# Performance work log

Hardware: AMD Instinct MI355X
Metric: run time of the kernel (lower is better)

Reference implementation:

```python
import jax, jax.numpy as jnp
import numpy as np


def _grid_sample_3d(vol, grid):
    """Trilinear 3D grid_sample, zero padding, align_corners=False (torch default).

    vol:  [B, C, D, H, W]
    grid: [B, P, 3] normalized coords in [-1, 1]; grid[...,0]->W axis,
          grid[...,1]->H axis, grid[...,2]->D axis (torch convention).
    returns [B, C, P]
    """
    B, C, D, H, W = vol.shape
    x = (grid[..., 0] + 1.0) * (W * 0.5) - 0.5
    y = (grid[..., 1] + 1.0) * (H * 0.5) - 0.5
    z = (grid[..., 2] + 1.0) * (D * 0.5) - 0.5
    x0, y0, z0 = jnp.floor(x), jnp.floor(y), jnp.floor(z)
    gather = jax.vmap(lambda v, zz, yy, xx: v[:, zz, yy, xx])  # per-batch gather -> [C, P]
    out = jnp.zeros((B, C, x.shape[1]), vol.dtype)
    for dz in (0.0, 1.0):
        for dy in (0.0, 1.0):
            for dx in (0.0, 1.0):
                xi, yi, zi = x0 + dx, y0 + dy, z0 + dz
                w = (1.0 - jnp.abs(x - xi)) * (1.0 - jnp.abs(y - yi)) * (1.0 - jnp.abs(z - zi))
                valid = (xi >= 0) & (xi < W) & (yi >= 0) & (yi < H) & (zi >= 0) & (zi < D)
                xc = jnp.clip(xi, 0, W - 1).astype(jnp.int32)
                yc = jnp.clip(yi, 0, H - 1).astype(jnp.int32)
                zc = jnp.clip(zi, 0, D - 1).astype(jnp.int32)
                vals = gather(vol, zc, yc, xc)  # [B, C, P]
                out = out + vals * jnp.where(valid, w, 0.0)[:, None, :]
    return out


def _offset_grid(xs, A, Wk):
    """xs: [N,3] sample points; A: [N,3,3]; Wk: [3,K] offset weights.
    Returns [N, K, 3] grid coords ordered (z_feat, y_feat, x_feat) as in the torch code."""
    off = jnp.einsum('nij,jk->nik', A, Wk)  # bmm with repeated weight -> [N,3,K]
    xf = xs[:, 2:3] + off[:, 0, :]
    yf = xs[:, 1:2] + off[:, 1, :]
    zf = xs[:, 0:1] + off[:, 2, :]
    return jnp.stack([zf, yf, xf], axis=-1)


def setup_inputs() -> dict:
    key = jax.random.key(0)
    k1, k2, k3, k4 = jax.random.split(key, 4)
    B, C, D, H, W = 2, 16, 96, 96, 96
    Feats, K = 512, 1024
    inp = jax.random.normal(k1, (B, C, D, H, W), jnp.float32)
    xyz_sample = jax.random.uniform(k2, (B, Feats, 3), jnp.float32, -1.0, 1.0)
    A = jax.random.normal(k3, (B * Feats, 3, 3), jnp.float32) * 0.1
    weight = jax.random.normal(k4, (6, K), jnp.float32) * 0.05  # xyz_off.weight
    return {"input": inp, "xyz_sample": xyz_sample, "A": A, "weight": weight}


def reference(input, xyz_sample, A, weight):
    B, Feats, _ = xyz_sample.shape
    C = input.shape[1]
    K = weight.shape[1]  # 1024
    xs = xyz_sample.reshape(B * Feats, 3)
    g1 = _offset_grid(xs, A, weight[:3]).reshape(B, Feats * K, 3)
    g2 = _offset_grid(xs, A, weight[3:]).reshape(B, Feats * K, 3)
    feats = _grid_sample_3d(input, g1) - _grid_sample_3d(input, g2)  # [B, C, Feats*K]
    return feats.reshape(B, C * Feats, K)
```

## Files before the change

### kernel.cpp

```cpp
#include <hip/hip_runtime.h>


#define NB 2
#define NC 16
#define NS 96
#define FEATS 512
#define NK 1024
#define KSPLIT 4
#define KSHIFT 2
#define KCHUNK (NK / KSPLIT)
#define PASSES (KCHUNK / 64)

#define TP 388

__device__ __forceinline__ unsigned int bfround(float f) {
  unsigned int u = __float_as_uint(f);
  return (u + 0x7fffu + ((u >> 16) & 1u)) >> 16;
}

__global__ __launch_bounds__(256) void transpose_bf16_kernel(
    const float* __restrict__ vol, unsigned short* __restrict__ volT) {
  int bid = blockIdx.x;
  int hq = bid % 24;
  int t = bid / 24;
  int d = t % NS;
  int b = t / NS;

  __shared__ float sm[NC * TP];
  int tid = threadIdx.x;

  const float4* v4 = (const float4*)vol;
#pragma unroll
  for (int j = 0; j < 6; j++) {
    int i = tid + 256 * j;
    int c = i / 96;
    int u = i - c * 96;
    size_t src = (size_t)((b * NC + c) * NS + d) * 2304 + hq * 96 + u;
    *(float4*)&sm[c * TP + u * 4] = v4[src];
  }
  __syncthreads();

  size_t dstb = ((size_t)(b * NS + d) * 9216 + (size_t)hq * 384) * NC;
#pragma unroll
  for (int j = 0; j < 3; j++) {
    int m = tid + 256 * j;
    int t16 = m >> 1;
    int ch = m & 1;
    unsigned int r[4];
#pragma unroll
    for (int q = 0; q < 4; q++) {
      float lo = sm[(ch * 8 + 2 * q) * TP + t16];
      float hi = sm[(ch * 8 + 2 * q + 1) * TP + t16];
      r[q] = bfround(lo) | (bfround(hi) << 16);
    }
    *(uint4*)(volT + dstb + (size_t)m * 8) = make_uint4(r[0], r[1], r[2], r[3]);
  }
}

__device__ __forceinline__ void tri_q_bf16(const unsigned short* __restrict__ vq,
                                           size_t bbase, float x, float y,
                                           float z, float sgn, float acc[4]) {
  float fx0 = floorf(x), fy0 = floorf(y), fz0 = floorf(z);
  int ix0 = (int)fx0, iy0 = (int)fy0, iz0 = (int)fz0;
  float tx = x - fx0, ty = y - fy0, tz = z - fz0;
  float wxa[2] = {1.0f - tx, tx};
  float wya[2] = {1.0f - ty, ty};
  float wza[2] = {1.0f - tz, tz};

#pragma unroll
  for (int dz = 0; dz < 2; dz++) {
    int zc = iz0 + dz;
    if ((unsigned)zc >= (unsigned)NS) continue;
#pragma unroll
    for (int dy = 0; dy < 2; dy++) {
      int yc = iy0 + dy;
      if ((unsigned)yc >= (unsigned)NS) continue;
      size_t rowb = bbase + ((size_t)zc * NS + yc) * (NS * NC);
      float wzy = sgn * wza[dz] * wya[dy];
#pragma unroll
      for (int dx = 0; dx < 2; dx++) {
        int xc = ix0 + dx;
        if ((unsigned)xc >= (unsigned)NS) continue;
        float w = wzy * wxa[dx];
        uint2 u = *(const uint2*)(vq + rowb + (size_t)xc * NC);
        acc[0] += w * __uint_as_float(u.x << 16);
        acc[1] += w * __uint_as_float(u.x & 0xffff0000u);
        acc[2] += w * __uint_as_float(u.y << 16);
        acc[3] += w * __uint_as_float(u.y & 0xffff0000u);
      }
    }
  }
}

__global__ __launch_bounds__(256) void sample_kernel_q(
    const unsigned short* __restrict__ volT,
    const float* __restrict__ xyz, const float* __restrict__ A,
    const float* __restrict__ weight, float* __restrict__ out) {
  __shared__ float wsm[6 * KCHUNK];

  int bid = blockIdx.x;
  int kseg = bid & (KSPLIT - 1);
  int n = bid >> KSHIFT;
  int b = n >> 9;
  int f = n & 511;
  int kbase = kseg * KCHUNK;

  for (int i = threadIdx.x; i < 6 * KCHUNK; i += 256)
    wsm[i] = weight[(i / KCHUNK) * NK + kbase + (i % KCHUNK)];

  const float* An = A + (size_t)n * 9;
  float a00 = An[0], a01 = An[1], a02 = An[2];
  float a10 = An[3], a11 = An[4], a12 = An[5];
  float a20 = An[6], a21 = An[7], a22 = An[8];
  const float* Xn = xyz + (size_t)n * 3;
  float bx = (Xn[0] + 1.0f) * 48.0f - 0.5f;
  float by = (Xn[1] + 1.0f) * 48.0f - 0.5f;
  float bz = (Xn[2] + 1.0f) * 48.0f - 0.5f;
  __syncthreads();

  int quad = threadIdx.x & 3;
  int ksub = threadIdx.x >> 2;
  const unsigned short* vq = volT + quad * 4;
  size_t bbase = (size_t)b * (NS * NS * NS * NC);
  size_t obase = (size_t)b * (NC * FEATS * NK) +
                 (size_t)(quad * 4) * (FEATS * NK) + (size_t)f * NK + kbase;

  for (int pass = 0; pass < PASSES; pass++) {
    int kl = pass * 64 + ksub;
    float w0 = wsm[kl];
    float w1 = wsm[KCHUNK + kl];
    float w2 = wsm[2 * KCHUNK + kl];
    float w3 = wsm[3 * KCHUNK + kl];
    float w4 = wsm[4 * KCHUNK + kl];
    float w5 = wsm[5 * KCHUNK + kl];

    float acc[4] = {0.0f, 0.0f, 0.0f, 0.0f};

    {
      float oz = a00 * w0 + a01 * w1 + a02 * w2;
      float oy = a10 * w0 + a11 * w1 + a12 * w2;
      float ox = a20 * w0 + a21 * w1 + a22 * w2;
      tri_q_bf16(vq, bbase, bx + ox * 48.0f, by + oy * 48.0f, bz + oz * 48.0f,
                 1.0f, acc);
    }
    {
      float oz = a00 * w3 + a01 * w4 + a02 * w5;
      float oy = a10 * w3 + a11 * w4 + a12 * w5;
      float ox = a20 * w3 + a21 * w4 + a22 * w5;
      tri_q_bf16(vq, bbase, bx + ox * 48.0f, by + oy * 48.0f, bz + oz * 48.0f,
                 -1.0f, acc);
    }

    size_t o = obase + kl;
    out[o] = acc[0];
    out[o + (size_t)(FEATS * NK)] = acc[1];
    out[o + 2 * (size_t)(FEATS * NK)] = acc[2];
    out[o + 3 * (size_t)(FEATS * NK)] = acc[3];
  }
}

__global__ __launch_bounds__(256) void sample_kernel_fallback(
    const float* __restrict__ vol, const float* __restrict__ xyz,
    const float* __restrict__ A, const float* __restrict__ weight,
    float* __restrict__ out) {
  int n = blockIdx.x;
  int b = n >> 9;
  int f = n & 511;
  const float* An = A + (size_t)n * 9;
  float a00 = An[0], a01 = An[1], a02 = An[2];
  float a10 = An[3], a11 = An[4], a12 = An[5];
  float a20 = An[6], a21 = An[7], a22 = An[8];
  const float* Xn = xyz + (size_t)n * 3;
  float bx = (Xn[0] + 1.0f) * 48.0f - 0.5f;
  float by = (Xn[1] + 1.0f) * 48.0f - 0.5f;
  float bz = (Xn[2] + 1.0f) * 48.0f - 0.5f;
  size_t obase = (size_t)b * (NC * FEATS * NK) + (size_t)f * NK;

  for (int k = threadIdx.x; k < NK; k += 256) {
    float w0 = weight[k], w1 = weight[NK + k], w2 = weight[2 * NK + k];
    float w3 = weight[3 * NK + k], w4 = weight[4 * NK + k],
          w5 = weight[5 * NK + k];
    float acc[NC];
#pragma unroll
    for (int c = 0; c < NC; c++) acc[c] = 0.0f;
    for (int g = 0; g < 2; g++) {
      float u0 = g ? w3 : w0, u1 = g ? w4 : w1, u2 = g ? w5 : w2;
      float sgn = g ? -1.0f : 1.0f;
      float oz = a00 * u0 + a01 * u1 + a02 * u2;
      float oy = a10 * u0 + a11 * u1 + a12 * u2;
      float ox = a20 * u0 + a21 * u1 + a22 * u2;
      float x = bx + ox * 48.0f, y = by + oy * 48.0f, z = bz + oz * 48.0f;
      float fx0 = floorf(x), fy0 = floorf(y), fz0 = floorf(z);
      int ix0 = (int)fx0, iy0 = (int)fy0, iz0 = (int)fz0;
      float tx = x - fx0, ty = y - fy0, tz = z - fz0;
      float wxa[2] = {1.0f - tx, tx}, wya[2] = {1.0f - ty, ty},
            wza[2] = {1.0f - tz, tz};
      for (int dz = 0; dz < 2; dz++) {
        int zc = iz0 + dz;
        if ((unsigned)zc >= (unsigned)NS) continue;
        for (int dy = 0; dy < 2; dy++) {
          int yc = iy0 + dy;
          if ((unsigned)yc >= (unsigned)NS) continue;
          for (int dx = 0; dx < 2; dx++) {
            int xc = ix0 + dx;
            if ((unsigned)xc >= (unsigned)NS) continue;
            float w = sgn * wza[dz] * wya[dy] * wxa[dx];
            size_t base = (size_t)b * NC * NS * NS * NS +
                          (size_t)zc * NS * NS + (size_t)yc * NS + xc;
#pragma unroll
            for (int c = 0; c < NC; c++)
              acc[c] += w * vol[base + (size_t)c * (NS * NS * NS)];
          }
        }
      }
    }
#pragma unroll
    for (int c = 0; c < NC; c++)
      out[obase + (size_t)c * (FEATS * NK) + k] = acc[c];
  }
}

extern "C" void kernel_launch(void* const* d_in, const int* in_sizes, int n_in,
                              void* d_out, int out_size, void* d_ws,
                              size_t ws_size, hipStream_t stream) {
  const float* vol    = (const float*)d_in[0];
  const float* xyz    = (const float*)d_in[1];
  const float* A      = (const float*)d_in[2];
  const float* weight = (const float*)d_in[3];
  float* out = (float*)d_out;

  const size_t volT_bytes =
      (size_t)NB * NC * NS * NS * NS * sizeof(unsigned short);

  if (ws_size >= volT_bytes) {
    unsigned short* volT = (unsigned short*)d_ws;
    transpose_bf16_kernel<<<NB * NS * 24, 256, 0, stream>>>(vol, volT);
    sample_kernel_q<<<NB * FEATS * KSPLIT, 256, 0, stream>>>(volT, xyz, A,
                                                             weight, out);
  } else {
    sample_kernel_fallback<<<NB * FEATS, 256, 0, stream>>>(vol, xyz, A, weight,
                                                           out);
  }
}
```

Before: 242.7 us.

## Replace full-volume bf16 transpose with per-block bounding-box LDS staging

```diff
diff --git a/kernel.cpp b/kernel.cpp
--- a/kernel.cpp
+++ b/kernel.cpp
@@ -10,56 +10,22 @@
 #define KSHIFT 2
 #define KCHUNK (NK / KSPLIT)
 #define PASSES (KCHUNK / 64)
-
-#define TP 388
+#define BOX 8
+#define VOXPAD 10
+#define PLANE (NS * NS)
+#define VOLC ((size_t)NS * NS * NS)
 
 __device__ __forceinline__ unsigned int bfround(float f) {
   unsigned int u = __float_as_uint(f);
   return (u + 0x7fffu + ((u >> 16) & 1u)) >> 16;
 }
-
-__global__ __launch_bounds__(256) void transpose_bf16_kernel(
-    const float* __restrict__ vol, unsigned short* __restrict__ volT) {
-  int bid = blockIdx.x;
-  int hq = bid % 24;
-  int t = bid / 24;
-  int d = t % NS;
-  int b = t / NS;
-
-  __shared__ float sm[NC * TP];
-  int tid = threadIdx.x;
-
-  const float4* v4 = (const float4*)vol;
-#pragma unroll
-  for (int j = 0; j < 6; j++) {
-    int i = tid + 256 * j;
-    int c = i / 96;
-    int u = i - c * 96;
-    size_t src = (size_t)((b * NC + c) * NS + d) * 2304 + hq * 96 + u;
-    *(float4*)&sm[c * TP + u * 4] = v4[src];
-  }
-  __syncthreads();
-
-  size_t dstb = ((size_t)(b * NS + d) * 9216 + (size_t)hq * 384) * NC;
-#pragma unroll
-  for (int j = 0; j < 3; j++) {
-    int m = tid + 256 * j;
-    int t16 = m >> 1;
-    int ch = m & 1;
-    unsigned int r[4];
-#pragma unroll
-    for (int q = 0; q < 4; q++) {
-      float lo = sm[(ch * 8 + 2 * q) * TP + t16];
-      float hi = sm[(ch * 8 + 2 * q + 1) * TP + t16];
-      r[q] = bfround(lo) | (bfround(hi) << 16);
-    }
-    *(uint4*)(volT + dstb + (size_t)m * 8) = make_uint4(r[0], r[1], r[2], r[3]);
-  }
-}
-
-__device__ __forceinline__ void tri_q_bf16(const unsigned short* __restrict__ vq,
-                                           size_t bbase, float x, float y,
-                                           float z, float sgn, float acc[4]) {
+__device__ __forceinline__ int imin(int a, int b) { return a < b ? a : b; }
+__device__ __forceinline__ int imax(int a, int b) { return a > b ? a : b; }
+
+__device__ __forceinline__ void tri_lds(const uint2* __restrict__ smq, int quad,
+                                        int ox, int oy, int oz, float x,
+                                        float y, float z, float sgn,
+                                        float acc[4]) {
   float fx0 = floorf(x), fy0 = floorf(y), fz0 = floorf(z);
   int ix0 = (int)fx0, iy0 = (int)fy0, iz0 = (int)fz0;
   float tx = x - fx0, ty = y - fy0, tz = z - fz0;
@@ -75,14 +41,15 @@
     for (int dy = 0; dy < 2; dy++) {
       int yc = iy0 + dy;
       if ((unsigned)yc >= (unsigned)NS) continue;
-      size_t rowb = bbase + ((size_t)zc * NS + yc) * (NS * NC);
+      int rowv = ((zc - oz) * BOX + (yc - oy)) * BOX;
       float wzy = sgn * wza[dz] * wya[dy];
 #pragma unroll
       for (int dx = 0; dx < 2; dx++) {
         int xc = ix0 + dx;
         if ((unsigned)xc >= (unsigned)NS) continue;
+        int vox = rowv + (xc - ox);
+        uint2 u = smq[vox * 5 + quad];
         float w = wzy * wxa[dx];
-        uint2 u = *(const uint2*)(vq + rowb + (size_t)xc * NC);
         acc[0] += w * __uint_as_float(u.x << 16);
         acc[1] += w * __uint_as_float(u.x & 0xffff0000u);
         acc[2] += w * __uint_as_float(u.y << 16);
@@ -92,11 +59,45 @@
   }
 }
 
-__global__ __launch_bounds__(256) void sample_kernel_q(
-    const unsigned short* __restrict__ volT,
-    const float* __restrict__ xyz, const float* __restrict__ A,
-    const float* __restrict__ weight, float* __restrict__ out) {
-  __shared__ float wsm[6 * KCHUNK];
+__device__ __forceinline__ void tri_glb(const float* __restrict__ vq, float x,
+                                        float y, float z, float sgn,
+                                        float acc[4]) {
+  float fx0 = floorf(x), fy0 = floorf(y), fz0 = floorf(z);
+  int ix0 = (int)fx0, iy0 = (int)fy0, iz0 = (int)fz0;
+  float tx = x - fx0, ty = y - fy0, tz = z - fz0;
+  float wxa[2] = {1.0f - tx, tx};
+  float wya[2] = {1.0f - ty, ty};
+  float wza[2] = {1.0f - tz, tz};
+
+#pragma unroll
+  for (int dz = 0; dz < 2; dz++) {
+    int zc = iz0 + dz;
+    if ((unsigned)zc >= (unsigned)NS) continue;
+#pragma unroll
+    for (int dy = 0; dy < 2; dy++) {
+      int yc = iy0 + dy;
+      if ((unsigned)yc >= (unsigned)NS) continue;
+      float wzy = sgn * wza[dz] * wya[dy];
+#pragma unroll
+      for (int dx = 0; dx < 2; dx++) {
+        int xc = ix0 + dx;
+        if ((unsigned)xc >= (unsigned)NS) continue;
+        float w = wzy * wxa[dx];
+        size_t p = (size_t)zc * PLANE + (size_t)yc * NS + xc;
+#pragma unroll
+        for (int i = 0; i < 4; i++) acc[i] += w * vq[p + (size_t)i * VOLC];
+      }
+    }
+  }
+}
+
+__global__ __launch_bounds__(256) void obelisk_kernel(
+    const float* __restrict__ vol, const float* __restrict__ xyz,
+    const float* __restrict__ A, const float* __restrict__ weight,
+    float* __restrict__ out) {
+  __shared__ unsigned int sm[BOX * BOX * BOX * VOXPAD];
+  __shared__ float red[4 * 6];
+  __shared__ int boxinfo[4];
 
   int bid = blockIdx.x;
   int kseg = bid & (KSPLIT - 1);
@@ -104,9 +105,6 @@
   int b = n >> 9;
   int f = n & 511;
   int kbase = kseg * KCHUNK;
-
-  for (int i = threadIdx.x; i < 6 * KCHUNK; i += 256)
-    wsm[i] = weight[(i / KCHUNK) * NK + kbase + (i % KCHUNK)];
 
   const float* An = A + (size_t)n * 9;
   float a00 = An[0], a01 = An[1], a02 = An[2];
@@ -116,39 +114,106 @@
   float bx = (Xn[0] + 1.0f) * 48.0f - 0.5f;
   float by = (Xn[1] + 1.0f) * 48.0f - 0.5f;
   float bz = (Xn[2] + 1.0f) * 48.0f - 0.5f;
+
+  float mnx, mny, mnz, mxx, mxy, mxz;
+  {
+    int k = kbase + threadIdx.x;
+    float w0 = weight[k], w1 = weight[NK + k], w2 = weight[2 * NK + k];
+    float w3 = weight[3 * NK + k], w4 = weight[4 * NK + k],
+          w5 = weight[5 * NK + k];
+    float x1 = bx + (a20 * w0 + a21 * w1 + a22 * w2) * 48.0f;
+    float y1 = by + (a10 * w0 + a11 * w1 + a12 * w2) * 48.0f;
+    float z1 = bz + (a00 * w0 + a01 * w1 + a02 * w2) * 48.0f;
+    float x2 = bx + (a20 * w3 + a21 * w4 + a22 * w5) * 48.0f;
+    float y2 = by + (a10 * w3 + a11 * w4 + a12 * w5) * 48.0f;
+    float z2 = bz + (a00 * w3 + a01 * w4 + a02 * w5) * 48.0f;
+    mnx = fminf(x1, x2); mxx = fmaxf(x1, x2);
+    mny = fminf(y1, y2); mxy = fmaxf(y1, y2);
+    mnz = fminf(z1, z2); mxz = fmaxf(z1, z2);
+  }
+#pragma unroll
+  for (int off = 32; off; off >>= 1) {
+    mnx = fminf(mnx, __shfl_xor(mnx, off));
+    mxx = fmaxf(mxx, __shfl_xor(mxx, off));
+    mny = fminf(mny, __shfl_xor(mny, off));
+    mxy = fmaxf(mxy, __shfl_xor(mxy, off));
+    mnz = fminf(mnz, __shfl_xor(mnz, off));
+    mxz = fmaxf(mxz, __shfl_xor(mxz, off));
+  }
+  int wid = threadIdx.x >> 6;
+  if ((threadIdx.x & 63) == 0) {
+    red[wid * 6 + 0] = mnx; red[wid * 6 + 1] = mxx;
+    red[wid * 6 + 2] = mny; red[wid * 6 + 3] = mxy;
+    red[wid * 6 + 4] = mnz; red[wid * 6 + 5] = mxz;
+  }
+  __syncthreads();
+  if (threadIdx.x == 0) {
+    float Mnx = red[0], Mxx = red[1], Mny = red[2], Mxy = red[3],
+          Mnz = red[4], Mxz = red[5];
+    for (int wv = 1; wv < 4; wv++) {
+      Mnx = fminf(Mnx, red[wv * 6 + 0]); Mxx = fmaxf(Mxx, red[wv * 6 + 1]);
+      Mny = fminf(Mny, red[wv * 6 + 2]); Mxy = fmaxf(Mxy, red[wv * 6 + 3]);
+      Mnz = fminf(Mnz, red[wv * 6 + 4]); Mxz = fmaxf(Mxz, red[wv * 6 + 5]);
+    }
+    int lox = imax(0, (int)floorf(Mnx)), hix = imin(NS - 1, (int)floorf(Mxx) + 1);
+    int loy = imax(0, (int)floorf(Mny)), hiy = imin(NS - 1, (int)floorf(Mxy) + 1);
+    int loz = imax(0, (int)floorf(Mnz)), hiz = imin(NS - 1, (int)floorf(Mxz) + 1);
+    int fb = (hix - lox > BOX - 1) | (hiy - loy > BOX - 1) | (hiz - loz > BOX - 1);
+    boxinfo[0] = imin(lox, NS - BOX);
+    boxinfo[1] = imin(loy, NS - BOX);
+    boxinfo[2] = imin(loz, NS - BOX);
+    boxinfo[3] = fb;
+  }
+  __syncthreads();
+  int ox = boxinfo[0], oy = boxinfo[1], oz = boxinfo[2], fb = boxinfo[3];
+
+  if (!fb) {
+    const float* vb = vol + (size_t)b * NC * VOLC;
+#pragma unroll
+    for (int j = 0; j < 16; j++) {
+      int idx = threadIdx.x + 256 * j;
+      int cpair = idx >> 9;
+      int vox = idx & 511;
+      int dx = vox & 7, dy = (vox >> 3) & 7, dz = vox >> 6;
+      size_t base = (size_t)(2 * cpair) * VOLC +
+                    (size_t)(oz + dz) * PLANE + (size_t)(oy + dy) * NS +
+                    (ox + dx);
+      float lo = vb[base];
+      float hi = vb[base + VOLC];
+      sm[vox * VOXPAD + cpair] = bfround(lo) | (bfround(hi) << 16);
+    }
+  }
   __syncthreads();
 
   int quad = threadIdx.x & 3;
   int ksub = threadIdx.x >> 2;
-  const unsigned short* vq = volT + quad * 4;
-  size_t bbase = (size_t)b * (NS * NS * NS * NC);
   size_t obase = (size_t)b * (NC * FEATS * NK) +
                  (size_t)(quad * 4) * (FEATS * NK) + (size_t)f * NK + kbase;
+  const uint2* smq = (const uint2*)sm;
+  const float* vq = vol + ((size_t)b * NC + quad * 4) * VOLC;
 
   for (int pass = 0; pass < PASSES; pass++) {
     int kl = pass * 64 + ksub;
-    float w0 = wsm[kl];
-    float w1 = wsm[KCHUNK + kl];
-    float w2 = wsm[2 * KCHUNK + kl];
-    float w3 = wsm[3 * KCHUNK + kl];
-    float w4 = wsm[4 * KCHUNK + kl];
-    float w5 = wsm[5 * KCHUNK + kl];
+    int k = kbase + kl;
+    float w0 = weight[k], w1 = weight[NK + k], w2 = weight[2 * NK + k];
+    float w3 = weight[3 * NK + k], w4 = weight[4 * NK + k],
+          w5 = weight[5 * NK + k];
 
     float acc[4] = {0.0f, 0.0f, 0.0f, 0.0f};
 
-    {
-      float oz = a00 * w0 + a01 * w1 + a02 * w2;
-      float oy = a10 * w0 + a11 * w1 + a12 * w2;
-      float ox = a20 * w0 + a21 * w1 + a22 * w2;
-      tri_q_bf16(vq, bbase, bx + ox * 48.0f, by + oy * 48.0f, bz + oz * 48.0f,
-                 1.0f, acc);
-    }
-    {
-      float oz = a00 * w3 + a01 * w4 + a02 * w5;
-      float oy = a10 * w3 + a11 * w4 + a12 * w5;
-      float ox = a20 * w3 + a21 * w4 + a22 * w5;
-      tri_q_bf16(vq, bbase, bx + ox * 48.0f, by + oy * 48.0f, bz + oz * 48.0f,
-                 -1.0f, acc);
+    float x1 = bx + (a20 * w0 + a21 * w1 + a22 * w2) * 48.0f;
+    float y1 = by + (a10 * w0 + a11 * w1 + a12 * w2) * 48.0f;
+    float z1 = bz + (a00 * w0 + a01 * w1 + a02 * w2) * 48.0f;
+    float x2 = bx + (a20 * w3 + a21 * w4 + a22 * w5) * 48.0f;
+    float y2 = by + (a10 * w3 + a11 * w4 + a12 * w5) * 48.0f;
+    float z2 = bz + (a00 * w3 + a01 * w4 + a02 * w5) * 48.0f;
+
+    if (!fb) {
+      tri_lds(smq, quad, ox, oy, oz, x1, y1, z1, 1.0f, acc);
+      tri_lds(smq, quad, ox, oy, oz, x2, y2, z2, -1.0f, acc);
+    } else {
+      tri_glb(vq, x1, y1, z1, 1.0f, acc);
+      tri_glb(vq, x2, y2, z2, -1.0f, acc);
     }
 
     size_t o = obase + kl;
@@ -156,67 +221,6 @@
     out[o + (size_t)(FEATS * NK)] = acc[1];
     out[o + 2 * (size_t)(FEATS * NK)] = acc[2];
     out[o + 3 * (size_t)(FEATS * NK)] = acc[3];
-  }
-}
-
-__global__ __launch_bounds__(256) void sample_kernel_fallback(
-    const float* __restrict__ vol, const float* __restrict__ xyz,
-    const float* __restrict__ A, const float* __restrict__ weight,
-    float* __restrict__ out) {
-  int n = blockIdx.x;
-  int b = n >> 9;
-  int f = n & 511;
-  const float* An = A + (size_t)n * 9;
-  float a00 = An[0], a01 = An[1], a02 = An[2];
-  float a10 = An[3], a11 = An[4], a12 = An[5];
-  float a20 = An[6], a21 = An[7], a22 = An[8];
-  const float* Xn = xyz + (size_t)n * 3;
-  float bx = (Xn[0] + 1.0f) * 48.0f - 0.5f;
-  float by = (Xn[1] + 1.0f) * 48.0f - 0.5f;
-  float bz = (Xn[2] + 1.0f) * 48.0f - 0.5f;
-  size_t obase = (size_t)b * (NC * FEATS * NK) + (size_t)f * NK;
-
-  for (int k = threadIdx.x; k < NK; k += 256) {
-    float w0 = weight[k], w1 = weight[NK + k], w2 = weight[2 * NK + k];
-    float w3 = weight[3 * NK + k], w4 = weight[4 * NK + k],
-          w5 = weight[5 * NK + k];
-    float acc[NC];
-#pragma unroll
-    for (int c = 0; c < NC; c++) acc[c] = 0.0f;
-    for (int g = 0; g < 2; g++) {
-      float u0 = g ? w3 : w0, u1 = g ? w4 : w1, u2 = g ? w5 : w2;
-      float sgn = g ? -1.0f : 1.0f;
-      float oz = a00 * u0 + a01 * u1 + a02 * u2;
-      float oy = a10 * u0 + a11 * u1 + a12 * u2;
-      float ox = a20 * u0 + a21 * u1 + a22 * u2;
-      float x = bx + ox * 48.0f, y = by + oy * 48.0f, z = bz + oz * 48.0f;
-      float fx0 = floorf(x), fy0 = floorf(y), fz0 = floorf(z);
-      int ix0 = (int)fx0, iy0 = (int)fy0, iz0 = (int)fz0;
-      float tx = x - fx0, ty = y - fy0, tz = z - fz0;
-      float wxa[2] = {1.0f - tx, tx}, wya[2] = {1.0f - ty, ty},
-            wza[2] = {1.0f - tz, tz};
-      for (int dz = 0; dz < 2; dz++) {
-        int zc = iz0 + dz;
-        if ((unsigned)zc >= (unsigned)NS) continue;
-        for (int dy = 0; dy < 2; dy++) {
-          int yc = iy0 + dy;
-          if ((unsigned)yc >= (unsigned)NS) continue;
-          for (int dx = 0; dx < 2; dx++) {
-            int xc = ix0 + dx;
-            if ((unsigned)xc >= (unsigned)NS) continue;
-            float w = sgn * wza[dz] * wya[dy] * wxa[dx];
-            size_t base = (size_t)b * NC * NS * NS * NS +
-                          (size_t)zc * NS * NS + (size_t)yc * NS + xc;
-#pragma unroll
-            for (int c = 0; c < NC; c++)
-              acc[c] += w * vol[base + (size_t)c * (NS * NS * NS)];
-          }
-        }
-      }
-    }
-#pragma unroll
-    for (int c = 0; c < NC; c++)
-      out[obase + (size_t)c * (FEATS * NK) + k] = acc[c];
   }
 }
 
@@ -228,17 +232,8 @@
   const float* A      = (const float*)d_in[2];
   const float* weight = (const float*)d_in[3];
   float* out = (float*)d_out;
-
-  const size_t volT_bytes =
-      (size_t)NB * NC * NS * NS * NS * sizeof(unsigned short);
-
-  if (ws_size >= volT_bytes) {
-    unsigned short* volT = (unsigned short*)d_ws;
-    transpose_bf16_kernel<<<NB * NS * 24, 256, 0, stream>>>(vol, volT);
-    sample_kernel_q<<<NB * FEATS * KSPLIT, 256, 0, stream>>>(volT, xyz, A,
-                                                             weight, out);
-  } else {
-    sample_kernel_fallback<<<NB * FEATS, 256, 0, stream>>>(vol, xyz, A, weight,
-                                                           out);
-  }
-}
+  (void)d_ws; (void)ws_size;
+
+  obelisk_kernel<<<NB * FEATS * KSPLIT, 256, 0, stream>>>(vol, xyz, A, weight,
+                                                          out);
+}
```

New measurement: 251.7 us. +3.7%, slower.
